# Kernel optimization log

Measured on AMD Instinct MI355X. Metric: run time of the kernel, lower is better.

The kernel has to match this reference:

```python
import jax, jax.numpy as jnp
import numpy as np

B, T, D = 4, 2048, 1024
H = 4                      # fla GatedLinearAttention default num_heads
K = D; V = D               # expand_k = expand_v = 1
DK = K // H; DV = V // H   # 256 each
LOW = 16                   # gate_low_rank_dim default
GLN = 16.0                 # gate_logit_normalizer default


def _layernorm(x, w, b, eps=1e-5):
    mu = x.mean(-1, keepdims=True)
    xc = x - mu
    var = (xc * xc).mean(-1, keepdims=True)
    return xc * jax.lax.rsqrt(var + eps) * w + b


def _rmsnorm(x, w, eps=1e-5):
    ms = (x * x).mean(-1, keepdims=True)
    return x * jax.lax.rsqrt(ms + eps) * w


def _gla_scan(q, k, v, gk):
    # q,k,gk: [B,T,H,DK]; v: [B,T,H,DV]
    scale = DK ** -0.5
    qT = jnp.moveaxis(q * scale, 1, 0)  # [T,B,H,DK]
    kT = jnp.moveaxis(k, 1, 0)
    vT = jnp.moveaxis(v, 1, 0)
    gT = jnp.moveaxis(gk, 1, 0)

    def step(h, inp):
        qt, kt, vt, gt = inp  # [B,H,DK]/[B,H,DV]
        h = h * jnp.exp(gt)[..., None] + kt[..., :, None] * vt[..., None, :]
        o = jnp.einsum('bhk,bhkv->bhv', qt, h)
        return h, o

    h0 = jnp.zeros((q.shape[0], H, DK, DV), q.dtype)
    _, oT = jax.lax.scan(step, h0, (qT, kT, vT, gT))
    return jnp.moveaxis(oT, 0, 1)  # [B,T,H,DV]


def setup_inputs() -> dict:
    key = jax.random.key(0)
    ks = jax.random.split(key, 12)
    rn = lambda k, s: jax.random.normal(k, s, jnp.float32) * 0.02
    return {
        'x': jax.random.normal(ks[0], (B, T, D), jnp.float32),
        'ln1_w': jnp.ones((D,), jnp.float32), 'ln1_b': jnp.zeros((D,), jnp.float32),
        'Wq': rn(ks[1], (D, K)), 'Wk': rn(ks[2], (D, K)), 'Wv': rn(ks[3], (D, V)),
        'Wg': rn(ks[4], (D, V)),
        'Wgk1': rn(ks[5], (D, LOW)), 'Wgk2': rn(ks[6], (LOW, K)), 'bgk2': jnp.zeros((K,), jnp.float32),
        'rms_w': jnp.ones((DV,), jnp.float32),
        'Wo': rn(ks[7], (V, D)),
        'ln2_w': jnp.ones((D,), jnp.float32), 'ln2_b': jnp.zeros((D,), jnp.float32),
        'W1': rn(ks[8], (D, 3 * D)), 'b1': jnp.zeros((3 * D,), jnp.float32),
        'W2': rn(ks[9], (3 * D, D)), 'b2': jnp.zeros((D,), jnp.float32),
    }


def reference(x, ln1_w, ln1_b, Wq, Wk, Wv, Wg, Wgk1, Wgk2, bgk2, rms_w, Wo,
              ln2_w, ln2_b, W1, b1, W2, b2):
    b, t = x.shape[0], x.shape[1]
    xn = _layernorm(x, ln1_w, ln1_b)
    q = (xn @ Wq).reshape(b, t, H, DK)
    k = (xn @ Wk).reshape(b, t, H, DK)
    v = (xn @ Wv).reshape(b, t, H, DV)
    # low-rank forget gate: logsigmoid / gate_logit_normalizer
    gk = (jax.nn.log_sigmoid((xn @ Wgk1) @ Wgk2 + bgk2) / GLN).reshape(b, t, H, DK)
    o = _gla_scan(q, k, v, gk)                      # [B,T,H,DV]
    g = (xn @ Wg).reshape(b, t, H, DV)              # output gate
    o = _rmsnorm(o, rms_w) * (g * jax.nn.sigmoid(g))  # gated RMSNorm (swish gate)
    o = o.reshape(b, t, V) @ Wo
    x = x + o
    xn2 = _layernorm(x, ln2_w, ln2_b)
    h = jax.nn.leaky_relu(xn2 @ W1 + b1, 0.01)
    h = h * h                                        # LeakyReLU^2
    x = x + (h @ W2 + b2)
    return x
```

## Files before the change

### kernel.cpp

```cpp
#include <hip/hip_runtime.h>
#include <math.h>

#define BB 4
#define TT 2048
#define DD 1024
#define HH 4
#define DK 256
#define DV 256
#define RR 8192
#define CHK 64
#define NCHK 32

typedef __bf16 bf16x8 __attribute__((ext_vector_type(8)));
typedef float f32x4 __attribute__((ext_vector_type(4)));

static __device__ inline unsigned short f2bf(float f) {
  unsigned int u = __float_as_uint(f);
  unsigned int r = (u + 0x7fffu + ((u >> 16) & 1u)) >> 16;
  return (unsigned short)r;
}
static __device__ inline float bf2f(unsigned short h) {
  return __uint_as_float(((unsigned int)h) << 16);
}

static __device__ __forceinline__ void gload16(const unsigned short* g,
                                               unsigned short* l) {
  __builtin_amdgcn_global_load_lds(
      (const __attribute__((address_space(1))) void*)g,
      (__attribute__((address_space(3))) void*)l, 16, 0, 0);
}

__global__ __launch_bounds__(256) void ln_kernel(const float* __restrict__ x,
                                                 const float* __restrict__ w,
                                                 const float* __restrict__ b,
                                                 unsigned short* __restrict__ yb) {
  int row = blockIdx.x;
  const float* xr = x + (size_t)row * DD;
  unsigned short* ybr = yb + (size_t)row * DD;
  int tid = threadIdx.x;

  float4 v = ((const float4*)xr)[tid];
  float s = v.x + v.y + v.z + v.w;
  float ss = v.x * v.x + v.y * v.y + v.z * v.z + v.w * v.w;
#pragma unroll
  for (int o = 32; o > 0; o >>= 1) {
    s += __shfl_down(s, o);
    ss += __shfl_down(ss, o);
  }
  __shared__ float ls[4], lss[4];
  int wid = tid >> 6;
  if ((tid & 63) == 0) { ls[wid] = s; lss[wid] = ss; }
  __syncthreads();
  float sum = ls[0] + ls[1] + ls[2] + ls[3];
  float sumsq = lss[0] + lss[1] + lss[2] + lss[3];
  float mu = sum * (1.0f / DD);
  float var = sumsq * (1.0f / DD) - mu * mu;
  float rs = rsqrtf(var + 1e-5f);

  float4 wv = ((const float4*)w)[tid];
  float4 bv = ((const float4*)b)[tid];
  ushort4 ob;
  ob.x = f2bf((v.x - mu) * rs * wv.x + bv.x);
  ob.y = f2bf((v.y - mu) * rs * wv.y + bv.y);
  ob.z = f2bf((v.z - mu) * rs * wv.z + bv.z);
  ob.w = f2bf((v.w - mu) * rs * wv.w + bv.w);
  ((ushort4*)ybr)[tid] = ob;
}

__global__ __launch_bounds__(256) void transpose_cast(const float* __restrict__ W,
                                                      unsigned short* __restrict__ Wt,
                                                      int K, int N) {
  __shared__ float t[32][33];
  int k0 = blockIdx.y * 32, n0 = blockIdx.x * 32;
  int tid = threadIdx.x;
  int tx = tid & 31, ty = tid >> 5;
#pragma unroll
  for (int i = 0; i < 4; ++i)
    t[ty + i * 8][tx] = W[(size_t)(k0 + ty + i * 8) * N + n0 + tx];
  __syncthreads();
#pragma unroll
  for (int i = 0; i < 4; ++i)
    Wt[(size_t)(n0 + ty + i * 8) * K + k0 + tx] = f2bf(t[tx][ty + i * 8]);
}

template <int EPI, int OUTBF>
__global__ __launch_bounds__(256) void gemm_bf16(
    const unsigned short* __restrict__ A,
    const unsigned short* __restrict__ Bt,
    const float* __restrict__ bias, const float* __restrict__ Res,
    void* __restrict__ Cv, int M, int N, int K) {
  __shared__ unsigned short As[128 * 64];
  __shared__ unsigned short Bs[128 * 64];
  int tid = threadIdx.x;
  int nwg = gridDim.x * gridDim.y;
  int wg = blockIdx.y * gridDim.x + blockIdx.x;
  int cpx = nwg >> 3;
  wg = (wg & 7) * cpx + (wg >> 3);
  int m0 = (wg / gridDim.x) * 128, n0 = (wg % gridDim.x) * 128;
  int lane = tid & 63;
  int w64 = tid & 192;
  int wid = tid >> 6;
  int wm = (wid >> 1) * 64, wn = (wid & 1) * 64;
  int fr = lane & 15, fq = lane >> 4;

  f32x4 acc[4][4] = {};

  for (int k0 = 0; k0 < K; k0 += 64) {
    __syncthreads();
#pragma unroll
    for (int j = 0; j < 4; ++j) {
      int gl = j * 256 + tid;
      int row = gl >> 3;
      int gs = (gl & 7) ^ (row & 7);
      gload16(&A[(size_t)(m0 + row) * K + k0 + gs * 8],
              &As[(size_t)(j * 256 + w64) * 8]);
      gload16(&Bt[(size_t)(n0 + row) * K + k0 + gs * 8],
              &Bs[(size_t)(j * 256 + w64) * 8]);
    }
    __syncthreads();

#pragma unroll
    for (int ph = 0; ph < 2; ++ph) {
      bf16x8 af[4], bv[4];
#pragma unroll
      for (int i = 0; i < 4; ++i) {
        int ra = wm + i * 16 + fr;
        af[i] = *(const bf16x8*)&As[ra * 64 + (((ph * 4 + fq) ^ (ra & 7)) * 8)];
        int rb = wn + i * 16 + fr;
        bv[i] = *(const bf16x8*)&Bs[rb * 64 + (((ph * 4 + fq) ^ (rb & 7)) * 8)];
      }
#pragma unroll
      for (int i = 0; i < 4; ++i)
#pragma unroll
        for (int jj = 0; jj < 4; ++jj)
          acc[i][jj] = __builtin_amdgcn_mfma_f32_16x16x32_bf16(af[i], bv[jj],
                                                               acc[i][jj], 0, 0, 0);
    }
  }

  int col = lane & 15;
  int rbase = (lane >> 4) * 4;
#pragma unroll
  for (int i = 0; i < 4; ++i) {
#pragma unroll
    for (int j = 0; j < 4; ++j) {
      int n = n0 + wn + j * 16 + col;
      float bvv = (EPI == 2 || EPI == 4) ? bias[n] : 0.0f;
#pragma unroll
      for (int r = 0; r < 4; ++r) {
        int m = m0 + wm + i * 16 + rbase + r;
        float vv = acc[i][j][r] + bvv;
        if (EPI == 2) {
          float t = vv > 0.0f ? vv : 0.01f * vv;
          vv = t * t;
        }
        if (EPI == 3 || EPI == 4) vv += Res[(size_t)m * N + n];
        if (OUTBF)
          ((unsigned short*)Cv)[(size_t)m * N + n] = f2bf(vv);
        else
          ((float*)Cv)[(size_t)m * N + n] = vv;
      }
    }
  }
}

__global__ __launch_bounds__(256) void gk_kernel(const unsigned short* __restrict__ xn,
                                                 const float* __restrict__ Wgk1,
                                                 const float* __restrict__ Wgk2,
                                                 const float* __restrict__ bgk2,
                                                 unsigned short* __restrict__ gk) {
  int row = blockIdx.x;
  const unsigned short* xr = xn + (size_t)row * DD;
  int tid = threadIdx.x;

  float t16[16];
#pragma unroll
  for (int j = 0; j < 16; ++j) t16[j] = 0.0f;

#pragma unroll
  for (int dd = 0; dd < 4; ++dd) {
    int d = tid + dd * 256;
    float xv = bf2f(xr[d]);
    const float4* wrow = (const float4*)(Wgk1 + (size_t)d * 16);
#pragma unroll
    for (int q = 0; q < 4; ++q) {
      float4 wq = wrow[q];
      t16[q * 4 + 0] += xv * wq.x;
      t16[q * 4 + 1] += xv * wq.y;
      t16[q * 4 + 2] += xv * wq.z;
      t16[q * 4 + 3] += xv * wq.w;
    }
  }
#pragma unroll
  for (int j = 0; j < 16; ++j) {
    float s = t16[j];
#pragma unroll
    for (int o = 32; o > 0; o >>= 1) s += __shfl_down(s, o);
    t16[j] = s;
  }
  __shared__ float tmp[4][16];
  __shared__ float tf[16];
  int wid = tid >> 6;
  if ((tid & 63) == 0) {
#pragma unroll
    for (int j = 0; j < 16; ++j) tmp[wid][j] = t16[j];
  }
  __syncthreads();
  if (tid < 16) tf[tid] = tmp[0][tid] + tmp[1][tid] + tmp[2][tid] + tmp[3][tid];
  __syncthreads();

  float tl[16];
#pragma unroll
  for (int j = 0; j < 16; ++j) tl[j] = tf[j];

#pragma unroll
  for (int jj = 0; jj < 4; ++jj) {
    int n = tid * 4 + jj;
    float z = bgk2[n];
#pragma unroll
    for (int j = 0; j < 16; ++j) z += tl[j] * Wgk2[j * 1024 + n];
    float ls = fminf(z, 0.0f) - log1pf(expf(-fabsf(z)));
    gk[(size_t)row * 1024 + n] = f2bf(ls * (1.0f / 16.0f));
  }
}

__global__ __launch_bounds__(256) void gate_chunk(const unsigned short* __restrict__ gk,
                                                  unsigned short* __restrict__ q,
                                                  unsigned short* __restrict__ k,
                                                  float* __restrict__ ebC) {
  int bid = blockIdx.x;
  int c = bid & 31;
  int h = (bid >> 5) & 3;
  int b = bid >> 7;
  int tid = threadIdx.x;
  size_t base = ((size_t)b * TT + c * CHK) * 1024 + h * 256 + tid;

  const float scale = 0.0625f;
  float cum = 0.0f;
  for (int t = 0; t < CHK; ++t) {
    size_t a = base + (size_t)t * 1024;
    cum += bf2f(gk[a]);
    q[a] = f2bf(bf2f(q[a]) * expf(cum) * scale);
    k[a] = f2bf(bf2f(k[a]) * expf(-cum));
  }
  ebC[((b * 4 + h) * NCHK + c) * 256 + tid] = expf(cum);
}

template <int WITHE>
__global__ __launch_bounds__(256) void trans_kernel(const unsigned short* __restrict__ in,
                                                    const float* __restrict__ ebC,
                                                    unsigned short* __restrict__ outT) {
  __shared__ unsigned short T[64][68];
  int bid = blockIdx.x;
  int dkt = bid & 3;
  int ct = (bid >> 2) & 31;
  int bh = bid >> 7;
  int b = bh >> 2, h = bh & 3;
  int tid = threadIdx.x;
  int r = tid >> 4;
  int c4 = (tid & 15) * 4;
  size_t srcbase = ((size_t)b * TT + ct * 64) * 1024 + h * 256 + dkt * 64;
#pragma unroll
  for (int i = 0; i < 4; ++i)
    *(ushort4*)&T[r + i * 16][c4] =
        *(const ushort4*)&in[srcbase + (size_t)(r + i * 16) * 1024 + c4];
  __syncthreads();
  size_t outbase = (size_t)bh * 524288 + (size_t)(dkt * 64) * 2048 + ct * 64;
  const float* ep = ebC + ((size_t)bh * 32 + ct) * 256 + dkt * 64;
#pragma unroll
  for (int i = 0; i < 4; ++i) {
    int dkl = r + i * 16;
    float e = WITHE ? ep[dkl] : 1.0f;
    ushort4 o;
    o.x = f2bf(bf2f(T[c4 + 0][dkl]) * e);
    o.y = f2bf(bf2f(T[c4 + 1][dkl]) * e);
    o.z = f2bf(bf2f(T[c4 + 2][dkl]) * e);
    o.w = f2bf(bf2f(T[c4 + 3][dkl]) * e);
    *(ushort4*)&outT[outbase + (size_t)dkl * 2048 + c4] = o;
  }
}

__global__ __launch_bounds__(256) void u_gemm(const unsigned short* __restrict__ khatT,
                                              const unsigned short* __restrict__ vT,
                                              unsigned short* __restrict__ UT) {
  __shared__ unsigned short As[128 * 64];
  __shared__ unsigned short Bs[128 * 64];
  int tid = threadIdx.x;
  int bid = blockIdx.x;
  int tile = bid & 3;
  int bhc = bid >> 2;
  int bh = bhc >> 5, c = bhc & 31;
  int m0 = (tile >> 1) * 128, n0 = (tile & 1) * 128;
  const unsigned short* Ab = vT + (size_t)bh * 524288 + c * 64;
  const unsigned short* Bb = khatT + (size_t)bh * 524288 + c * 64;
  unsigned short* Cb = UT + (size_t)bhc * 65536;

  int lane = tid & 63;
  int w64 = tid & 192;
  int wid = tid >> 6;
  int wm = (wid >> 1) * 64, wn = (wid & 1) * 64;
  int fr = lane & 15, fq = lane >> 4;

  f32x4 acc[4][4] = {};

#pragma unroll
  for (int j = 0; j < 4; ++j) {
    int gl = j * 256 + tid;
    int row = gl >> 3;
    int gs = (gl & 7) ^ (row & 7);
    gload16(&Ab[(size_t)(m0 + row) * 2048 + gs * 8],
            &As[(size_t)(j * 256 + w64) * 8]);
    gload16(&Bb[(size_t)(n0 + row) * 2048 + gs * 8],
            &Bs[(size_t)(j * 256 + w64) * 8]);
  }
  __syncthreads();

#pragma unroll
  for (int ph = 0; ph < 2; ++ph) {
    bf16x8 af[4], bv[4];
#pragma unroll
    for (int i = 0; i < 4; ++i) {
      int ra = wm + i * 16 + fr;
      af[i] = *(const bf16x8*)&As[ra * 64 + (((ph * 4 + fq) ^ (ra & 7)) * 8)];
      int rb = wn + i * 16 + fr;
      bv[i] = *(const bf16x8*)&Bs[rb * 64 + (((ph * 4 + fq) ^ (rb & 7)) * 8)];
    }
#pragma unroll
    for (int i = 0; i < 4; ++i)
#pragma unroll
      for (int jj = 0; jj < 4; ++jj)
        acc[i][jj] = __builtin_amdgcn_mfma_f32_16x16x32_bf16(af[i], bv[jj],
                                                             acc[i][jj], 0, 0, 0);
  }

  int col = lane & 15;
  int rbase = (lane >> 4) * 4;
#pragma unroll
  for (int i = 0; i < 4; ++i)
#pragma unroll
    for (int j = 0; j < 4; ++j) {
      int n = n0 + wn + j * 16 + col;
#pragma unroll
      for (int r = 0; r < 4; ++r) {
        int m = m0 + wm + i * 16 + rbase + r;
        Cb[(size_t)m * 256 + n] = f2bf(acc[i][j][r]);
      }
    }
}

__global__ __launch_bounds__(256) void hscan(unsigned short* __restrict__ UH,
                                             const float* __restrict__ ebC) {
  int bid = blockIdx.x;
  int bh = bid >> 8, dv = bid & 255;
  int tid = threadIdx.x;
  size_t base = ((size_t)bh * NCHK) * 65536 + (size_t)dv * 256 + tid;
  const float* ebb = ebC + (size_t)bh * NCHK * 256;
  float h = 0.0f;
  for (int c = 0; c < NCHK; ++c) {
    size_t a = base + (size_t)c * 65536;
    float u = bf2f(UH[a]);
    UH[a] = f2bf(h);
    h = ebb[c * 256 + tid] * h + u;
  }
}

__global__ __launch_bounds__(256) void intra_mfma(
    const unsigned short* __restrict__ qt, const unsigned short* __restrict__ kt,
    const unsigned short* __restrict__ vT, float* __restrict__ o) {
  __shared__ unsigned short QK[2][64 * 264];
  __shared__ unsigned short Sb[64 * 64];
  unsigned short* Vs = &QK[0][0];

  int bid = blockIdx.x;
  int c = bid & 31;
  int bh = bid >> 5;
  int b = bh >> 2, h = bh & 3;
  size_t rowbase = ((size_t)b * TT + c * 64) * 1024 + h * 256;
  size_t vtbase = (size_t)bh * 524288 + c * 64;
  int tid = threadIdx.x;
  int lane = tid & 63;
  int w = tid >> 6;
  int fr = lane & 15, fq = lane >> 4;

#pragma unroll
  for (int i = 0; i < 8; ++i) {
    int g = tid + i * 256;
    int row = g >> 5, gc = g & 31;
    *(bf16x8*)&QK[0][row * 264 + gc * 8] =
        *(const bf16x8*)&qt[rowbase + (size_t)row * 1024 + gc * 8];
    *(bf16x8*)&QK[1][row * 264 + gc * 8] =
        *(const bf16x8*)&kt[rowbase + (size_t)row * 1024 + gc * 8];
  }
  __syncthreads();

  {
    f32x4 accs[4] = {};
#pragma unroll
    for (int ks = 0; ks < 8; ++ks) {
      bf16x8 af = *(const bf16x8*)&QK[0][(w * 16 + fr) * 264 + ks * 32 + fq * 8];
#pragma unroll
      for (int si = 0; si < 4; ++si) {
        bf16x8 bf_ = *(const bf16x8*)&QK[1][(si * 16 + fr) * 264 + ks * 32 + fq * 8];
        accs[si] = __builtin_amdgcn_mfma_f32_16x16x32_bf16(af, bf_, accs[si], 0, 0, 0);
      }
    }
#pragma unroll
    for (int si = 0; si < 4; ++si) {
#pragma unroll
      for (int r = 0; r < 4; ++r) {
        int t = w * 16 + fq * 4 + r;
        int s = si * 16 + fr;
        float val = (s <= t) ? accs[si][r] : 0.0f;
        int gS = s >> 3;
        Sb[t * 64 + ((gS ^ (t & 7)) * 8) + (s & 7)] = f2bf(val);
      }
    }
  }
  __syncthreads();

#pragma unroll
  for (int i = 0; i < 8; ++i) {
    int g = tid + i * 256;
    int dv = g >> 3, gc = g & 7;
    *(bf16x8*)&Vs[dv * 72 + gc * 8] =
        *(const bf16x8*)&vT[vtbase + (size_t)dv * 2048 + gc * 8];
  }
  __syncthreads();

  {
    int dv0 = w * 64;
    f32x4 acco[4][4] = {};
#pragma unroll
    for (int ks = 0; ks < 2; ++ks) {
      bf16x8 af[4], bv[4];
#pragma unroll
      for (int ti = 0; ti < 4; ++ti) {
        int t = ti * 16 + fr;
        af[ti] = *(const bf16x8*)&Sb[t * 64 + (((ks * 4 + fq) ^ (t & 7)) * 8)];
      }
#pragma unroll
      for (int nj = 0; nj < 4; ++nj)
        bv[nj] = *(const bf16x8*)&Vs[(dv0 + nj * 16 + fr) * 72 + ks * 32 + fq * 8];
#pragma unroll
      for (int ti = 0; ti < 4; ++ti)
#pragma unroll
        for (int nj = 0; nj < 4; ++nj)
          acco[ti][nj] = __builtin_amdgcn_mfma_f32_16x16x32_bf16(af[ti], bv[nj],
                                                                 acco[ti][nj], 0, 0, 0);
    }
#pragma unroll
    for (int ti = 0; ti < 4; ++ti)
#pragma unroll
      for (int nj = 0; nj < 4; ++nj)
#pragma unroll
        for (int r = 0; r < 4; ++r) {
          int t = ti * 16 + fq * 4 + r;
          int dv = dv0 + nj * 16 + fr;
          o[rowbase + (size_t)t * 1024 + dv] = acco[ti][nj][r];
        }
  }
}

__global__ __launch_bounds__(256) void inter_mfma(
    const unsigned short* __restrict__ qt, const unsigned short* __restrict__ HT,
    float* __restrict__ o) {
  __shared__ unsigned short Qs[64 * 264];
  __shared__ unsigned short Hs[256 * 72];
  int bid = blockIdx.x;
  int c = bid & 31;
  int bh = bid >> 5;
  int b = bh >> 2, h = bh & 3;
  size_t rowbase = ((size_t)b * TT + c * 64) * 1024 + h * 256;
  size_t htbase = ((size_t)(bh * 32 + c)) * 65536;
  int tid = threadIdx.x;
  int lane = tid & 63;
  int w = tid >> 6;
  int fr = lane & 15, fq = lane >> 4;
  int dv0 = w * 64;

#pragma unroll
  for (int i = 0; i < 8; ++i) {
    int g = tid + i * 256;
    int row = g >> 5, gc = g & 31;
    *(bf16x8*)&Qs[row * 264 + gc * 8] =
        *(const bf16x8*)&qt[rowbase + (size_t)row * 1024 + gc * 8];
  }

  f32x4 acc[4][4] = {};
  for (int k4 = 0; k4 < 4; ++k4) {
    __syncthreads();
#pragma unroll
    for (int i = 0; i < 8; ++i) {
      int g = tid + i * 256;
      int dv = g >> 3, gc = g & 7;
      *(bf16x8*)&Hs[dv * 72 + gc * 8] =
          *(const bf16x8*)&HT[htbase + (size_t)dv * 256 + k4 * 64 + gc * 8];
    }
    __syncthreads();
#pragma unroll
    for (int ks = 0; ks < 2; ++ks) {
      bf16x8 af[4], bv[4];
#pragma unroll
      for (int ti = 0; ti < 4; ++ti)
        af[ti] = *(const bf16x8*)&Qs[(ti * 16 + fr) * 264 + k4 * 64 + ks * 32 + fq * 8];
#pragma unroll
      for (int nj = 0; nj < 4; ++nj)
        bv[nj] = *(const bf16x8*)&Hs[(dv0 + nj * 16 + fr) * 72 + ks * 32 + fq * 8];
#pragma unroll
      for (int ti = 0; ti < 4; ++ti)
#pragma unroll
        for (int nj = 0; nj < 4; ++nj)
          acc[ti][nj] = __builtin_amdgcn_mfma_f32_16x16x32_bf16(af[ti], bv[nj],
                                                                acc[ti][nj], 0, 0, 0);
    }
  }

#pragma unroll
  for (int ti = 0; ti < 4; ++ti)
#pragma unroll
    for (int nj = 0; nj < 4; ++nj)
#pragma unroll
      for (int r = 0; r < 4; ++r) {
        int t = ti * 16 + fq * 4 + r;
        int dv = dv0 + nj * 16 + fr;
        size_t a = rowbase + (size_t)t * 1024 + dv;
        o[a] += acc[ti][nj][r];
      }
}

__global__ __launch_bounds__(256) void grms_kernel(const float* __restrict__ o,
                                                   const unsigned short* __restrict__ g,
                                                   const float* __restrict__ rw,
                                                   unsigned short* __restrict__ og) {
  size_t base = (size_t)blockIdx.x * 256;
  int tid = threadIdx.x;
  float ov = o[base + tid];
  float s = ov * ov;
#pragma unroll
  for (int off = 32; off > 0; off >>= 1) s += __shfl_down(s, off);
  __shared__ float red[4];
  int wid = tid >> 6;
  if ((tid & 63) == 0) red[wid] = s;
  __syncthreads();
  float ms = (red[0] + red[1] + red[2] + red[3]) * (1.0f / 256.0f);
  float gv = bf2f(g[base + tid]);
  float sw = gv / (1.0f + expf(-gv));
  og[base + tid] = f2bf(ov * rsqrtf(ms + 1e-5f) * rw[tid] * sw);
}

extern "C" void kernel_launch(void* const* d_in, const int* in_sizes, int n_in,
                              void* d_out, int out_size, void* d_ws,
                              size_t ws_size, hipStream_t stream) {
  const float* x = (const float*)d_in[0];
  const float* ln1_w = (const float*)d_in[1];
  const float* ln1_b = (const float*)d_in[2];
  const float* Wq = (const float*)d_in[3];
  const float* Wk = (const float*)d_in[4];
  const float* Wv = (const float*)d_in[5];
  const float* Wg = (const float*)d_in[6];
  const float* Wgk1 = (const float*)d_in[7];
  const float* Wgk2 = (const float*)d_in[8];
  const float* bgk2 = (const float*)d_in[9];
  const float* rms_w = (const float*)d_in[10];
  const float* Wo = (const float*)d_in[11];
  const float* ln2_w = (const float*)d_in[12];
  const float* ln2_b = (const float*)d_in[13];
  const float* W1 = (const float*)d_in[14];
  const float* b1 = (const float*)d_in[15];
  const float* W2 = (const float*)d_in[16];
  const float* b2 = (const float*)d_in[17];
  float* out = (float*)d_out;

  const size_t S = (size_t)RR * DD;
  unsigned short* actb = (unsigned short*)d_ws;
  unsigned short* qb = actb + S;
  unsigned short* kb = qb + S;
  unsigned short* vb = kb + S;
  unsigned short* gb = vb + S;
  unsigned short* gkb = gb + S;
  float* ofs = (float*)(gkb + S);
  unsigned short* UH = (unsigned short*)(ofs + S);
  float* ebC = (float*)(UH + 4 * S);
  unsigned short* Wqt = (unsigned short*)(ebC + 131072);
  unsigned short* Wkt = Wqt + 1048576;
  unsigned short* Wvt = Wkt + 1048576;
  unsigned short* Wgt = Wvt + 1048576;
  unsigned short* Wot = Wgt + 1048576;
  unsigned short* W1t = Wot + 1048576;
  unsigned short* W2t = W1t + 3145728;
  unsigned short* khatT = gkb;
  unsigned short* vT = actb;
  float* x1 = (float*)kb;
  unsigned short* hb = UH;

  dim3 blk(256);

  transpose_cast<<<dim3(32, 32), blk, 0, stream>>>(Wq, Wqt, 1024, 1024);
  transpose_cast<<<dim3(32, 32), blk, 0, stream>>>(Wk, Wkt, 1024, 1024);
  transpose_cast<<<dim3(32, 32), blk, 0, stream>>>(Wv, Wvt, 1024, 1024);
  transpose_cast<<<dim3(32, 32), blk, 0, stream>>>(Wg, Wgt, 1024, 1024);
  transpose_cast<<<dim3(32, 32), blk, 0, stream>>>(Wo, Wot, 1024, 1024);
  transpose_cast<<<dim3(96, 32), blk, 0, stream>>>(W1, W1t, 1024, 3072);
  transpose_cast<<<dim3(32, 96), blk, 0, stream>>>(W2, W2t, 3072, 1024);

  ln_kernel<<<RR, blk, 0, stream>>>(x, ln1_w, ln1_b, actb);

  dim3 g1024(1024 / 128, RR / 128);
  gemm_bf16<0, 1><<<g1024, blk, 0, stream>>>(actb, Wqt, nullptr, nullptr, qb, RR, 1024, 1024);
  gemm_bf16<0, 1><<<g1024, blk, 0, stream>>>(actb, Wkt, nullptr, nullptr, kb, RR, 1024, 1024);
  gemm_bf16<0, 1><<<g1024, blk, 0, stream>>>(actb, Wvt, nullptr, nullptr, vb, RR, 1024, 1024);
  gemm_bf16<0, 1><<<g1024, blk, 0, stream>>>(actb, Wgt, nullptr, nullptr, gb, RR, 1024, 1024);

  gk_kernel<<<RR, blk, 0, stream>>>(actb, Wgk1, Wgk2, bgk2, gkb);

  gate_chunk<<<BB * HH * NCHK, blk, 0, stream>>>(gkb, qb, kb, ebC);

  trans_kernel<1><<<16 * 32 * 4, blk, 0, stream>>>(kb, ebC, khatT);
  trans_kernel<0><<<16 * 32 * 4, blk, 0, stream>>>(vb, ebC, vT);

  u_gemm<<<16 * NCHK * 4, blk, 0, stream>>>(khatT, vT, UH);
  hscan<<<16 * 256, blk, 0, stream>>>(UH, ebC);

  intra_mfma<<<16 * NCHK, blk, 0, stream>>>(qb, kb, vT, ofs);
  inter_mfma<<<16 * NCHK, blk, 0, stream>>>(qb, UH, ofs);

  grms_kernel<<<RR * HH, blk, 0, stream>>>(ofs, gb, rms_w, actb);

  gemm_bf16<3, 0><<<g1024, blk, 0, stream>>>(actb, Wot, nullptr, x, x1, RR, 1024, 1024);

  ln_kernel<<<RR, blk, 0, stream>>>(x1, ln2_w, ln2_b, actb);

  dim3 g3072(3072 / 128, RR / 128);
  gemm_bf16<2, 1><<<g3072, blk, 0, stream>>>(actb, W1t, b1, nullptr, hb, RR, 3072, 1024);

  gemm_bf16<4, 0><<<g1024, blk, 0, stream>>>(hb, W2t, b2, x1, out, RR, 1024, 3072);
}
```

Baseline: 497.6 us.

## Double-buffer GEMM LDS tiles and fuse Q/K/V/G projections into one GEMM

```diff
diff --git a/kernel.cpp b/kernel.cpp
--- a/kernel.cpp
+++ b/kernel.cpp
@@ -10,6 +10,7 @@
 #define RR 8192
 #define CHK 64
 #define NCHK 32
+#define SS ((size_t)RR * DD)
 
 typedef __bf16 bf16x8 __attribute__((ext_vector_type(8)));
 typedef float f32x4 __attribute__((ext_vector_type(4)));
@@ -89,8 +90,8 @@
     const unsigned short* __restrict__ Bt,
     const float* __restrict__ bias, const float* __restrict__ Res,
     void* __restrict__ Cv, int M, int N, int K) {
-  __shared__ unsigned short As[128 * 64];
-  __shared__ unsigned short Bs[128 * 64];
+  __shared__ unsigned short As[2][128 * 64];
+  __shared__ unsigned short Bs[2][128 * 64];
   int tid = threadIdx.x;
   int nwg = gridDim.x * gridDim.y;
   int wg = blockIdx.y * gridDim.x + blockIdx.x;
@@ -105,19 +106,26 @@
 
   f32x4 acc[4][4] = {};
 
-  for (int k0 = 0; k0 < K; k0 += 64) {
-    __syncthreads();
+  auto STAGE = [&](int buf, int k0) {
 #pragma unroll
     for (int j = 0; j < 4; ++j) {
       int gl = j * 256 + tid;
       int row = gl >> 3;
       int gs = (gl & 7) ^ (row & 7);
       gload16(&A[(size_t)(m0 + row) * K + k0 + gs * 8],
-              &As[(size_t)(j * 256 + w64) * 8]);
+              &As[buf][(size_t)(j * 256 + w64) * 8]);
       gload16(&Bt[(size_t)(n0 + row) * K + k0 + gs * 8],
-              &Bs[(size_t)(j * 256 + w64) * 8]);
-    }
-    __syncthreads();
+              &Bs[buf][(size_t)(j * 256 + w64) * 8]);
+    }
+  };
+
+  STAGE(0, 0);
+  asm volatile("s_waitcnt vmcnt(0)");
+  __syncthreads();
+
+  int cur = 0;
+  for (int k0 = 0; k0 < K; k0 += 64) {
+    if (k0 + 64 < K) STAGE(cur ^ 1, k0 + 64);
 
 #pragma unroll
     for (int ph = 0; ph < 2; ++ph) {
@@ -125,9 +133,9 @@
 #pragma unroll
       for (int i = 0; i < 4; ++i) {
         int ra = wm + i * 16 + fr;
-        af[i] = *(const bf16x8*)&As[ra * 64 + (((ph * 4 + fq) ^ (ra & 7)) * 8)];
+        af[i] = *(const bf16x8*)&As[cur][ra * 64 + (((ph * 4 + fq) ^ (ra & 7)) * 8)];
         int rb = wn + i * 16 + fr;
-        bv[i] = *(const bf16x8*)&Bs[rb * 64 + (((ph * 4 + fq) ^ (rb & 7)) * 8)];
+        bv[i] = *(const bf16x8*)&Bs[cur][rb * 64 + (((ph * 4 + fq) ^ (rb & 7)) * 8)];
       }
 #pragma unroll
       for (int i = 0; i < 4; ++i)
@@ -136,6 +144,8 @@
           acc[i][jj] = __builtin_amdgcn_mfma_f32_16x16x32_bf16(af[i], bv[jj],
                                                                acc[i][jj], 0, 0, 0);
     }
+    __syncthreads();
+    cur ^= 1;
   }
 
   int col = lane & 15;
@@ -155,10 +165,14 @@
           vv = t * t;
         }
         if (EPI == 3 || EPI == 4) vv += Res[(size_t)m * N + n];
-        if (OUTBF)
+        if (EPI == 5) {
+          ((unsigned short*)Cv)[(size_t)(n >> 10) * SS + (size_t)m * 1024 +
+                                (n & 1023)] = f2bf(vv);
+        } else if (OUTBF) {
           ((unsigned short*)Cv)[(size_t)m * N + n] = f2bf(vv);
-        else
+        } else {
           ((float*)Cv)[(size_t)m * N + n] = vv;
+        }
       }
     }
   }
@@ -571,7 +585,7 @@
   const float* b2 = (const float*)d_in[17];
   float* out = (float*)d_out;
 
-  const size_t S = (size_t)RR * DD;
+  const size_t S = SS;
   unsigned short* actb = (unsigned short*)d_ws;
   unsigned short* qb = actb + S;
   unsigned short* kb = qb + S;
@@ -581,11 +595,8 @@
   float* ofs = (float*)(gkb + S);
   unsigned short* UH = (unsigned short*)(ofs + S);
   float* ebC = (float*)(UH + 4 * S);
-  unsigned short* Wqt = (unsigned short*)(ebC + 131072);
-  unsigned short* Wkt = Wqt + 1048576;
-  unsigned short* Wvt = Wkt + 1048576;
-  unsigned short* Wgt = Wvt + 1048576;
-  unsigned short* Wot = Wgt + 1048576;
+  unsigned short* Wqkvgt = (unsigned short*)(ebC + 131072);
+  unsigned short* Wot = Wqkvgt + 4194304;
   unsigned short* W1t = Wot + 1048576;
   unsigned short* W2t = W1t + 3145728;
   unsigned short* khatT = gkb;
@@ -595,21 +606,19 @@
 
   dim3 blk(256);
 
-  transpose_cast<<<dim3(32, 32), blk, 0, stream>>>(Wq, Wqt, 1024, 1024);
-  transpose_cast<<<dim3(32, 32), blk, 0, stream>>>(Wk, Wkt, 1024, 1024);
-  transpose_cast<<<dim3(32, 32), blk, 0, stream>>>(Wv, Wvt, 1024, 1024);
-  transpose_cast<<<dim3(32, 32), blk, 0, stream>>>(Wg, Wgt, 1024, 1024);
+  transpose_cast<<<dim3(32, 32), blk, 0, stream>>>(Wq, Wqkvgt, 1024, 1024);
+  transpose_cast<<<dim3(32, 32), blk, 0, stream>>>(Wk, Wqkvgt + 1048576, 1024, 1024);
+  transpose_cast<<<dim3(32, 32), blk, 0, stream>>>(Wv, Wqkvgt + 2097152, 1024, 1024);
+  transpose_cast<<<dim3(32, 32), blk, 0, stream>>>(Wg, Wqkvgt + 3145728, 1024, 1024);
   transpose_cast<<<dim3(32, 32), blk, 0, stream>>>(Wo, Wot, 1024, 1024);
   transpose_cast<<<dim3(96, 32), blk, 0, stream>>>(W1, W1t, 1024, 3072);
   transpose_cast<<<dim3(32, 96), blk, 0, stream>>>(W2, W2t, 3072, 1024);
 
   ln_kernel<<<RR, blk, 0, stream>>>(x, ln1_w, ln1_b, actb);
 
-  dim3 g1024(1024 / 128, RR / 128);
-  gemm_bf16<0, 1><<<g1024, blk, 0, stream>>>(actb, Wqt, nullptr, nullptr, qb, RR, 1024, 1024);
-  gemm_bf16<0, 1><<<g1024, blk, 0, stream>>>(actb, Wkt, nullptr, nullptr, kb, RR, 1024, 1024);
-  gemm_bf16<0, 1><<<g1024, blk, 0, stream>>>(actb, Wvt, nullptr, nullptr, vb, RR, 1024, 1024);
-  gemm_bf16<0, 1><<<g1024, blk, 0, stream>>>(actb, Wgt, nullptr, nullptr, gb, RR, 1024, 1024);
+  dim3 g4096(4096 / 128, RR / 128);
+  gemm_bf16<5, 1><<<g4096, blk, 0, stream>>>(actb, Wqkvgt, nullptr, nullptr, qb,
+                                             RR, 4096, 1024);
 
   gk_kernel<<<RR, blk, 0, stream>>>(actb, Wgk1, Wgk2, bgk2, gkb);
 
@@ -626,6 +635,7 @@
 
   grms_kernel<<<RR * HH, blk, 0, stream>>>(ofs, gb, rms_w, actb);
 
+  dim3 g1024(1024 / 128, RR / 128);
   gemm_bf16<3, 0><<<g1024, blk, 0, stream>>>(actb, Wot, nullptr, x, x1, RR, 1024, 1024);
 
   ln_kernel<<<RR, blk, 0, stream>>>(x1, ln2_w, ln2_b, actb);
```

Measured after the change: 474.4 us. -4.7%, faster.
